# Kernel optimization log

Measured on AMD Instinct MI355X. Metric: run time of the kernel, lower is better.

Reference implementation:

```python
import jax, jax.numpy as jnp
import numpy as np

EPS = 1e-7  # keras.backend.epsilon()


def setup_inputs() -> dict:
    key = jax.random.key(0)
    kx, kw, ku = jax.random.split(key, 3)
    B, S, F = 16, 4096, 512
    x = jax.random.normal(kx, (B, S, F), dtype=jnp.float32)
    # glorot-uniform-scaled weights
    limW = np.sqrt(6.0 / (F + F)).astype(np.float32)
    W = jax.random.uniform(kw, (F, F), dtype=jnp.float32, minval=-limW, maxval=limW)
    b = jnp.zeros((F,), dtype=jnp.float32)
    limu = np.sqrt(6.0 / (F + 1)).astype(np.float32)
    u = jax.random.uniform(ku, (F,), dtype=jnp.float32, minval=-limu, maxval=limu)
    return {"x": x, "W": W, "b": b, "u": u}


def reference(x, W, b, u):
    # x: [B,S,F]  W: [F,F]  b: [F]  u: [F]
    h = jnp.tanh(jnp.einsum('bsf,fg->bsg', x, W) + b)   # [B,S,F]
    scores = jnp.einsum('bsf,f->bs', h, u)              # [B,S]
    e = jnp.exp(scores)
    # NOTE: faithful to the source, normalization is GLOBAL over all B*S scores
    a = e / (jnp.sum(e) + EPS)                          # [B,S]
    out = jnp.einsum('bsf,bs->bf', x, a)                # [B,F] weighted-sum pool over steps
    return out
```

## Files before the change

kernel.cpp:

```cpp
#include <hip/hip_runtime.h>
#include <stdint.h>

#define EPSV 1e-7f
#define FDIM 512
#define ROWS 64
#define NROWS 65536
#define NBLK (NROWS / ROWS)

typedef __bf16 bf16_t;
typedef bf16_t bf16x8 __attribute__((ext_vector_type(8)));
typedef unsigned short ushort8 __attribute__((ext_vector_type(8)));
typedef float f32x4 __attribute__((ext_vector_type(4)));

__device__ __forceinline__ unsigned short f2bf(float f) {
  union { float f; unsigned int u; } c; c.f = f;
  unsigned int u = c.u;
  unsigned int r = u + 0x7fffu + ((u >> 16) & 1u);
  return (unsigned short)(r >> 16);
}
__device__ __forceinline__ float bf2f(unsigned short s) {
  union { unsigned int u; float f; } c; c.u = ((unsigned int)s) << 16;
  return c.f;
}

__device__ __forceinline__ float fast_tanh(float x) {
  x = fminf(15.0f, fmaxf(-15.0f, x));
  float t = __expf(2.0f * x);
  return 1.0f - 2.0f * __builtin_amdgcn_rcpf(t + 1.0f);
}

__global__ void convert_W(const float* __restrict__ W, unsigned short* __restrict__ Wt2,
                          float* __restrict__ sumE) {
  if (blockIdx.x == 0 && threadIdx.x == 0) *sumE = 0.0f;
  __shared__ unsigned short tile[32][34];
  const int t = threadIdx.x;
  const int tx = t & 31, ty = t >> 5;
  const int bn = blockIdx.x & 15, bk = blockIdx.x >> 4;
  const int k0 = bk * 32, n0 = bn * 32;
#pragma unroll
  for (int i = 0; i < 4; ++i) {
    int r = ty + i * 8;
    tile[r][tx] = f2bf(W[(size_t)(k0 + r) * FDIM + n0 + tx]);
  }
  __syncthreads();
#pragma unroll
  for (int i = 0; i < 4; ++i) {
    int r = ty + i * 8;
    Wt2[(size_t)(k0 >> 5) * (FDIM * 32) + (size_t)(n0 + r) * 32 + tx] = tile[tx][r];
  }
}

__global__ __launch_bounds__(512, 4) void fused_score_pool(
    const float* __restrict__ x, const unsigned short* __restrict__ Wt2,
    const float* __restrict__ bvec, const float* __restrict__ uvec,
    float* __restrict__ ppool, float* __restrict__ sumE) {
  __shared__ alignas(16) unsigned short sA[ROWS * FDIM];
  __shared__ float score_s[ROWS];
  __shared__ float e_s[ROWS];

  const int t = threadIdx.x;
  const int lane = t & 63;
  const int w = t >> 6;
  const int quad = lane >> 4;
  const int l15 = lane & 15;
  const int m0 = blockIdx.x * ROWS;

  if (t < ROWS) score_s[t] = 0.0f;

#pragma unroll
  for (int p = 0; p < 8; ++p) {
    const int row = p * 8 + w;
    const float* g = x + (size_t)(m0 + row) * FDIM + lane * 8;
    float4 lo = *(const float4*)g;
    float4 hi = *(const float4*)(g + 4);
    ushort8 v;
    v[0] = f2bf(lo.x); v[1] = f2bf(lo.y); v[2] = f2bf(lo.z); v[3] = f2bf(lo.w);
    v[4] = f2bf(hi.x); v[5] = f2bf(hi.y); v[6] = f2bf(hi.z); v[7] = f2bf(hi.w);
    const int jp = lane ^ (row & 7);
    *(ushort8*)(void*)(sA + row * FDIM + jp * 8) = v;
  }
  __syncthreads();

  f32x4 acc[4][4];
#pragma unroll
  for (int mi = 0; mi < 4; ++mi)
#pragma unroll
    for (int ni = 0; ni < 4; ++ni) acc[mi][ni] = (f32x4){0.f, 0.f, 0.f, 0.f};

  const unsigned short* bp = Wt2 + (size_t)(w * 64 + l15) * 32 + quad * 8;

#pragma unroll 2
  for (int kc = 0; kc < 16; ++kc) {
    bf16x8 bfr[4], af[4];
#pragma unroll
    for (int ni = 0; ni < 4; ++ni)
      bfr[ni] = *(const bf16x8*)(const void*)(bp + (size_t)kc * (FDIM * 32) + ni * 512);
#pragma unroll
    for (int mi = 0; mi < 4; ++mi) {
      const int row = mi * 16 + l15;
      const int phys = (kc * 4 + quad) ^ (row & 7);
      af[mi] = *(const bf16x8*)(const void*)(sA + row * FDIM + phys * 8);
    }
    __builtin_amdgcn_s_setprio(1);
#pragma unroll
    for (int mi = 0; mi < 4; ++mi)
#pragma unroll
      for (int ni = 0; ni < 4; ++ni)
        acc[mi][ni] = __builtin_amdgcn_mfma_f32_16x16x32_bf16(
            af[mi], bfr[ni], acc[mi][ni], 0, 0, 0);
    __builtin_amdgcn_s_setprio(0);
  }

  float uu[4], bb[4];
#pragma unroll
  for (int ni = 0; ni < 4; ++ni) {
    const int cl = w * 64 + ni * 16 + l15;
    uu[ni] = uvec[cl];
    bb[ni] = bvec[cl];
  }
#pragma unroll
  for (int mi = 0; mi < 4; ++mi)
#pragma unroll
    for (int r = 0; r < 4; ++r) {
      float v = 0.0f;
#pragma unroll
      for (int ni = 0; ni < 4; ++ni)
        v += uu[ni] * fast_tanh(acc[mi][ni][r] + bb[ni]);
      v += __shfl_xor(v, 1); v += __shfl_xor(v, 2);
      v += __shfl_xor(v, 4); v += __shfl_xor(v, 8);
      if (l15 == 0)
        atomicAdd(&score_s[mi * 16 + quad * 4 + r], v);
    }
  __syncthreads();

  if (t < ROWS) {
    const float e = __expf(score_s[t]);
    e_s[t] = e;
    float v = e;
    v += __shfl_xor(v, 1);  v += __shfl_xor(v, 2);  v += __shfl_xor(v, 4);
    v += __shfl_xor(v, 8);  v += __shfl_xor(v, 16); v += __shfl_xor(v, 32);
    if (lane == 0) atomicAdd(sumE, v);
  }
  __syncthreads();

  {
    const int col = t;
    const int jblk = col >> 3, jj = col & 7;
    float s = 0.0f;
#pragma unroll 8
    for (int row = 0; row < ROWS; ++row) {
      const int phys = ((jblk ^ (row & 7)) << 3) + jj;
      s += bf2f(sA[row * FDIM + phys]) * e_s[row];
    }
    ppool[(size_t)blockIdx.x * FDIM + col] = s;
  }
}

__global__ __launch_bounds__(256) void finalize(
    const float* __restrict__ ppool, const float* __restrict__ sumE,
    float* __restrict__ out) {
  const int i = blockIdx.x * 256 + threadIdx.x;
  const int b = i >> 9, f = i & 511;
  const float* p = ppool + (size_t)b * 64 * FDIM + f;
  float s = 0.0f;
#pragma unroll
  for (int c = 0; c < 64; ++c) s += p[(size_t)c * FDIM];
  out[i] = s / (*sumE + EPSV);
}

extern "C" void kernel_launch(void* const* d_in, const int* in_sizes, int n_in,
                              void* d_out, int out_size, void* d_ws, size_t ws_size,
                              hipStream_t stream) {
  (void)in_sizes; (void)n_in; (void)out_size; (void)ws_size;
  const float* x = (const float*)d_in[0];
  const float* W = (const float*)d_in[1];
  const float* b = (const float*)d_in[2];
  const float* u = (const float*)d_in[3];
  float* out = (float*)d_out;

  char* p = (char*)d_ws;
  unsigned short* Wt2 = (unsigned short*)p;  p += (size_t)FDIM * FDIM * 2;
  float* sumE = (float*)p;                   p += 256;
  float* ppool = (float*)p;                  p += (size_t)NBLK * FDIM * 4;

  convert_W<<<dim3(256), dim3(256), 0, stream>>>(W, Wt2, sumE);
  fused_score_pool<<<dim3(NBLK), dim3(512), 0, stream>>>(
      x, Wt2, b, u, ppool, sumE);
  finalize<<<dim3(32), dim3(256), 0, stream>>>(ppool, sumE, out);
}
```

Baseline: 236.5 us.

## Halve rows per block and double-buffer W fragment loads across K steps

Each block now handles 32 rows instead of 64, which halves the shared-memory tile and accumulator registers and doubles the block count. W fragments are prefetched in a two-register ping-pong, and the first load is issued before the x staging, so global B loads overlap the MFMAs. The cost is twice as many reads of W from L2 and twice as many partial-pool rows for finalize to sum. It also adds register pressure from the extra B buffers.

```diff
diff --git a/kernel.cpp b/kernel.cpp
--- a/kernel.cpp
+++ b/kernel.cpp
@@ -3,7 +3,7 @@
 
 #define EPSV 1e-7f
 #define FDIM 512
-#define ROWS 64
+#define ROWS 32
 #define NROWS 65536
 #define NBLK (NROWS / ROWS)
 
@@ -67,8 +67,20 @@
 
   if (t < ROWS) score_s[t] = 0.0f;
 
-#pragma unroll
-  for (int p = 0; p < 8; ++p) {
+  const unsigned short* bp = Wt2 + (size_t)(w * 64 + l15) * 32 + quad * 8;
+
+#define LOADB(dst_, kc_)                                                       \
+  do {                                                                         \
+    _Pragma("unroll") for (int ni_ = 0; ni_ < 4; ++ni_)                        \
+        dst_[ni_] = *(const bf16x8*)(const void*)(                             \
+            bp + (size_t)(kc_) * (FDIM * 32) + ni_ * 512);                     \
+  } while (0)
+
+  bf16x8 bA[4], bB[4];
+  LOADB(bA, 0);
+
+#pragma unroll
+  for (int p = 0; p < 4; ++p) {
     const int row = p * 8 + w;
     const float* g = x + (size_t)(m0 + row) * FDIM + lane * 8;
     float4 lo = *(const float4*)g;
@@ -81,34 +93,35 @@
   }
   __syncthreads();
 
-  f32x4 acc[4][4];
-#pragma unroll
-  for (int mi = 0; mi < 4; ++mi)
+  f32x4 acc[2][4];
+#pragma unroll
+  for (int mi = 0; mi < 2; ++mi)
 #pragma unroll
     for (int ni = 0; ni < 4; ++ni) acc[mi][ni] = (f32x4){0.f, 0.f, 0.f, 0.f};
 
-  const unsigned short* bp = Wt2 + (size_t)(w * 64 + l15) * 32 + quad * 8;
-
-#pragma unroll 2
-  for (int kc = 0; kc < 16; ++kc) {
-    bf16x8 bfr[4], af[4];
-#pragma unroll
-    for (int ni = 0; ni < 4; ++ni)
-      bfr[ni] = *(const bf16x8*)(const void*)(bp + (size_t)kc * (FDIM * 32) + ni * 512);
-#pragma unroll
-    for (int mi = 0; mi < 4; ++mi) {
-      const int row = mi * 16 + l15;
-      const int phys = (kc * 4 + quad) ^ (row & 7);
-      af[mi] = *(const bf16x8*)(const void*)(sA + row * FDIM + phys * 8);
-    }
-    __builtin_amdgcn_s_setprio(1);
-#pragma unroll
-    for (int mi = 0; mi < 4; ++mi)
-#pragma unroll
-      for (int ni = 0; ni < 4; ++ni)
-        acc[mi][ni] = __builtin_amdgcn_mfma_f32_16x16x32_bf16(
-            af[mi], bfr[ni], acc[mi][ni], 0, 0, 0);
-    __builtin_amdgcn_s_setprio(0);
+#define MFMA_STEP(bcur_, kc_)                                                  \
+  do {                                                                         \
+    bf16x8 af_[2];                                                             \
+    _Pragma("unroll") for (int mi_ = 0; mi_ < 2; ++mi_) {                      \
+      const int row_ = mi_ * 16 + l15;                                         \
+      const int phys_ = ((kc_) * 4 + quad) ^ (row_ & 7);                       \
+      af_[mi_] = *(const bf16x8*)(const void*)(sA + row_ * FDIM + phys_ * 8);  \
+    }                                                                          \
+    __builtin_amdgcn_s_setprio(1);                                             \
+    _Pragma("unroll") for (int mi_ = 0; mi_ < 2; ++mi_)                        \
+        _Pragma("unroll") for (int ni_ = 0; ni_ < 4; ++ni_)                    \
+            acc[mi_][ni_] = __builtin_amdgcn_mfma_f32_16x16x32_bf16(           \
+                af_[mi_], bcur_[ni_], acc[mi_][ni_], 0, 0, 0);                 \
+    __builtin_amdgcn_s_setprio(0);                                             \
+  } while (0)
+
+#pragma unroll
+  for (int kc2 = 0; kc2 < 8; ++kc2) {
+    const int kc = kc2 * 2;
+    LOADB(bB, kc + 1);
+    MFMA_STEP(bA, kc);
+    LOADB(bA, (kc + 2) & 15);
+    MFMA_STEP(bB, kc + 1);
   }
 
   float uu[4], bb[4];
@@ -119,7 +132,7 @@
     bb[ni] = bvec[cl];
   }
 #pragma unroll
-  for (int mi = 0; mi < 4; ++mi)
+  for (int mi = 0; mi < 2; ++mi)
 #pragma unroll
     for (int r = 0; r < 4; ++r) {
       float v = 0.0f;
@@ -138,7 +151,7 @@
     e_s[t] = e;
     float v = e;
     v += __shfl_xor(v, 1);  v += __shfl_xor(v, 2);  v += __shfl_xor(v, 4);
-    v += __shfl_xor(v, 8);  v += __shfl_xor(v, 16); v += __shfl_xor(v, 32);
+    v += __shfl_xor(v, 8);  v += __shfl_xor(v, 16);
     if (lane == 0) atomicAdd(sumE, v);
   }
   __syncthreads();
@@ -161,10 +174,10 @@
     float* __restrict__ out) {
   const int i = blockIdx.x * 256 + threadIdx.x;
   const int b = i >> 9, f = i & 511;
-  const float* p = ppool + (size_t)b * 64 * FDIM + f;
+  const float* p = ppool + (size_t)b * 128 * FDIM + f;
   float s = 0.0f;
 #pragma unroll
-  for (int c = 0; c < 64; ++c) s += p[(size_t)c * FDIM];
+  for (int c = 0; c < 128; ++c) s += p[(size_t)c * FDIM];
   out[i] = s / (*sumE + EPSV);
 }
 
```

New measurement: 263.6 us. +11.5%, slower.
